# Performance work log

Measured on AMD Instinct MI355X. Metric: run time of the kernel, lower is better.

Reference implementation:

```python
import jax, jax.numpy as jnp
import numpy as np

N_NODES = 8192
N_EDGES = 524288
D_IN = 256
D_OUT = 256


def setup_inputs() -> dict:
    key = jax.random.key(0)
    ks = jax.random.split(key, 8)
    h = jax.random.normal(ks[0], (N_NODES, D_IN), dtype=jnp.float32)
    # Xavier-uniform-like scale for weights
    s = (6.0 / (D_IN + D_OUT)) ** 0.5
    W = jax.random.uniform(ks[1], (D_IN, D_OUT), jnp.float32, -s, s)
    Wq = jax.random.uniform(ks[2], (D_IN, D_OUT), jnp.float32, -s, s)
    bq = jnp.zeros((D_OUT,), jnp.float32)
    Wk = jax.random.uniform(ks[3], (D_IN, D_OUT), jnp.float32, -s, s)
    bk = jnp.zeros((D_OUT,), jnp.float32)
    senders = jax.random.randint(ks[4], (N_EDGES,), 0, N_NODES, dtype=jnp.int64 if jax.config.jax_enable_x64 else jnp.int32)
    receivers = jax.random.randint(ks[5], (N_EDGES,), 0, N_NODES, dtype=jnp.int64 if jax.config.jax_enable_x64 else jnp.int32)
    return {"h": h, "W": W, "Wq": Wq, "bq": bq, "Wk": Wk, "bk": bk,
            "senders": senders, "receivers": receivers}


def reference(h, W, Wq, bq, Wk, bk, senders, receivers):
    # Projected node features: (N, D_OUT)
    h_proj = jnp.dot(h, W)
    # Dense attention logits a = q @ k^T: (N, N), as in the original module
    q = jnp.dot(h, Wq) + bq
    k = jnp.dot(h, Wk) + bk
    a = jnp.dot(q, k.T)
    # Gather per-edge messages and attention weights, weight, scatter-add
    messages = h_proj[senders] * a[senders, receivers][:, None]  # (E, D_OUT)
    aggregated = jax.ops.segment_sum(messages, receivers, num_segments=h.shape[0])
    return jax.nn.relu(aggregated)
```

## Files before the change

kernel.cpp:

```cpp
#include <hip/hip_runtime.h>
#include <stdint.h>

typedef unsigned short u16;
typedef unsigned int u32;
typedef short v8s __attribute__((ext_vector_type(8)));
typedef float v4f __attribute__((ext_vector_type(4)));

#define N_NODES 8192
#define N_EDGES 524288
#define DFEAT 256
#define PAD 160

static __device__ __forceinline__ float bflo(u32 u) { return __uint_as_float(u << 16); }
static __device__ __forceinline__ float bfhi(u32 u) { return __uint_as_float(u & 0xffff0000u); }
static __device__ __forceinline__ u16 f2bf(float f) {
    u32 u = __float_as_uint(f);
    u32 r = (u + 0x7fffu + ((u >> 16) & 1u)) >> 16;
    return (u16)r;
}

__global__ void prep(const float* __restrict__ h,
                     const float* __restrict__ w0, const float* __restrict__ w1,
                     const float* __restrict__ w2,
                     const int* __restrict__ recv, const int* __restrict__ send,
                     u16* __restrict__ hb, u16* __restrict__ wt,
                     int* __restrict__ cnt, int* __restrict__ es_pad) {
    __shared__ u16 t[64][65];
    int b = blockIdx.x;
    if (b < 2048) {
        int i = (b * 256 + threadIdx.x) * 4;
        float4 v = *(const float4*)(h + i);
        uint2 p;
        p.x = (u32)f2bf(v.x) | ((u32)f2bf(v.y) << 16);
        p.y = (u32)f2bf(v.z) | ((u32)f2bf(v.w) << 16);
        *(uint2*)(hb + i) = p;
    } else if (b < 2096) {
        int bb = b - 2048;
        int region = bb >> 4;
        int tile = bb & 15;
        int k0 = (tile >> 2) * 64, n0 = (tile & 3) * 64;
        const float* w = (region == 0) ? w0 : ((region == 1) ? w1 : w2);
        int tx = threadIdx.x & 63, ty = threadIdx.x >> 6;
#pragma unroll
        for (int it = 0; it < 16; it++) {
            int row = it * 4 + ty;
            t[row][tx] = f2bf(w[(k0 + row) * 256 + n0 + tx]);
        }
        __syncthreads();
        u16* o = wt + region * 65536;
#pragma unroll
        for (int it = 0; it < 16; it++) {
            int row = it * 4 + ty;
            o[(n0 + row) * 256 + k0 + tx] = t[tx][row];
        }
    } else {
        int e = (b - 2096) * 256 + threadIdx.x;
        int r = recv[e];
        int pos = atomicAdd(&cnt[r], 1);
        if (pos < PAD) es_pad[r * PAD + pos] = send[e];
    }
}

__global__ __launch_bounds__(256) void gemm_proj(
    const u16* __restrict__ h, const u16* __restrict__ wt,
    const float* __restrict__ bq, const float* __restrict__ bk,
    u16* __restrict__ hproj, u16* __restrict__ qb, u16* __restrict__ kb) {
    int wave = threadIdx.x >> 6;
    int lane = threadIdx.x & 63;
    int lm = lane & 15;
    int lq = lane >> 4;
    int m0 = blockIdx.x * 64 + wave * 16;
    int region = blockIdx.y >> 2;
    int n0b = (blockIdx.y & 3) * 64;
    const u16* wtr = wt + region * 65536;

    v4f acc[4];
#pragma unroll
    for (int nt = 0; nt < 4; nt++) acc[nt] = (v4f){0.f, 0.f, 0.f, 0.f};

    const u16* arow = h + (m0 + lm) * 256 + lq * 8;
#pragma unroll
    for (int k0 = 0; k0 < 256; k0 += 32) {
        v8s a = *(const v8s*)(arow + k0);
#pragma unroll
        for (int nt = 0; nt < 4; nt++) {
            v8s b = *(const v8s*)(wtr + (n0b + nt * 16 + lm) * 256 + k0 + lq * 8);
            acc[nt] = __builtin_amdgcn_mfma_f32_16x16x32_bf16(a, b, acc[nt], 0, 0, 0);
        }
    }

    u16* outp = (region == 0) ? hproj : ((region == 1) ? qb : kb);
    const float* bias = (region == 1) ? bq : ((region == 2) ? bk : nullptr);
#pragma unroll
    for (int nt = 0; nt < 4; nt++) {
        int n = n0b + nt * 16 + lm;
        float bv = bias ? bias[n] : 0.f;
#pragma unroll
        for (int i = 0; i < 4; i++) {
            int m = m0 + lq * 4 + i;
            outp[m * 256 + n] = f2bf(acc[nt][i] + bv);
        }
    }
}

__global__ __launch_bounds__(256) void edge_fused(
    const u16* __restrict__ qb, const u16* __restrict__ kb, const u16* __restrict__ hpb,
    const int* __restrict__ cnt, const int* __restrict__ es_pad,
    float* __restrict__ out) {
    __shared__ float sc[4][16];
    __shared__ int   ss[4][16];
    int wave = threadIdx.x >> 6;
    int lane = threadIdx.x & 63;
    int r = blockIdx.x * 4 + wave;
    int lm = lane & 15, lq = lane >> 4;
    int lh = lane & 31, half = lane >> 5;
    int colbase = lh * 8;
    int n = min(cnt[r], PAD);
    int base = r * PAD;

    v8s kf[8];
    const u16* krow = kb + r * 256 + lq * 8;
#pragma unroll
    for (int t = 0; t < 8; t++) kf[t] = *(const v8s*)(krow + t * 32);

    float a[8];
#pragma unroll
    for (int i = 0; i < 8; i++) a[i] = 0.f;

    for (int c0 = 0; c0 < n; c0 += 16) {
        int j = c0 + lm;
        if (j >= n) j = n - 1;
        int s = es_pad[base + j];
        const u16* qrow = qb + s * 256 + lq * 8;
        v4f acc = (v4f){0.f, 0.f, 0.f, 0.f};
#pragma unroll
        for (int t = 0; t < 8; t++) {
            v8s av = *(const v8s*)(qrow + t * 32);
            acc = __builtin_amdgcn_mfma_f32_16x16x32_bf16(av, kf[t], acc, 0, 0, 0);
        }
        if (lm == 0) {
#pragma unroll
            for (int i = 0; i < 4; i++) sc[wave][lq * 4 + i] = acc[i];
        }
        if (lq == 0) ss[wave][lm] = s;
        __threadfence_block();

        int m = n - c0;
        if (m >= 16) {
#pragma unroll
            for (int t0 = 0; t0 < 8; t0++) {
                int t = t0 * 2 + half;
                float p = sc[wave][t];
                int s2 = ss[wave][t];
                uint4 hv = *(const uint4*)(hpb + s2 * 256 + colbase);
                a[0] += p * bflo(hv.x); a[1] += p * bfhi(hv.x);
                a[2] += p * bflo(hv.y); a[3] += p * bfhi(hv.y);
                a[4] += p * bflo(hv.z); a[5] += p * bfhi(hv.z);
                a[6] += p * bflo(hv.w); a[7] += p * bfhi(hv.w);
            }
        } else {
            for (int t = half; t < m; t += 2) {
                float p = sc[wave][t];
                int s2 = ss[wave][t];
                uint4 hv = *(const uint4*)(hpb + s2 * 256 + colbase);
                a[0] += p * bflo(hv.x); a[1] += p * bfhi(hv.x);
                a[2] += p * bflo(hv.y); a[3] += p * bfhi(hv.y);
                a[4] += p * bflo(hv.z); a[5] += p * bfhi(hv.z);
                a[6] += p * bflo(hv.w); a[7] += p * bfhi(hv.w);
            }
        }
    }

#pragma unroll
    for (int i = 0; i < 8; i++) a[i] += __shfl_xor(a[i], 32, 64);

    if (half == 0) {
        float4 o0, o1;
        o0.x = fmaxf(a[0], 0.f); o0.y = fmaxf(a[1], 0.f);
        o0.z = fmaxf(a[2], 0.f); o0.w = fmaxf(a[3], 0.f);
        o1.x = fmaxf(a[4], 0.f); o1.y = fmaxf(a[5], 0.f);
        o1.z = fmaxf(a[6], 0.f); o1.w = fmaxf(a[7], 0.f);
        float* op = out + r * 256 + colbase;
        *(float4*)op = o0;
        *(float4*)(op + 4) = o1;
    }
}

extern "C" void kernel_launch(void* const* d_in, const int* in_sizes, int n_in,
                              void* d_out, int out_size, void* d_ws, size_t ws_size,
                              hipStream_t stream) {
    const float* h  = (const float*)d_in[0];
    const float* W  = (const float*)d_in[1];
    const float* Wq = (const float*)d_in[2];
    const float* bq = (const float*)d_in[3];
    const float* Wk = (const float*)d_in[4];
    const float* bk = (const float*)d_in[5];
    const int* senders   = (const int*)d_in[6];
    const int* receivers = (const int*)d_in[7];
    float* out = (float*)d_out;

    char* ws = (char*)d_ws;
    u16* wt     = (u16*)ws;
    u16* hb     = (u16*)(ws + 393216);
    u16* hproj  = hb + N_NODES * DFEAT;
    u16* qb     = hproj + N_NODES * DFEAT;
    u16* kb     = qb + N_NODES * DFEAT;
    int* cnt    = (int*)(kb + N_NODES * DFEAT);
    int* es_pad = cnt + N_NODES;

    hipMemsetAsync(cnt, 0, N_NODES * sizeof(int), stream);
    prep<<<4144, 256, 0, stream>>>(h, W, Wq, Wk, receivers, senders, hb, wt, cnt, es_pad);
    gemm_proj<<<dim3(128, 12), 256, 0, stream>>>(hb, wt, bq, bk, hproj, qb, kb);
    edge_fused<<<N_NODES / 4, 256, 0, stream>>>(qb, kb, hproj, cnt, es_pad, out);
}
```

Measured before the change: 181.5 us.

## Restructure pipeline: fuse bucketing with GEMM, drop memset, scalar edge dot products

The memset is replaced by zeroing inside a small weight-transpose kernel. The edge bucketing is merged into the projection GEMM launch, and the GEMM now converts fp32 h to bf16 on the fly instead of using a separate hb buffer. Sender indices are stored as 16-bit values in the padded bucket array, and the edge kernel computes each q·k dot product with per-lane FMAs and shuffle reductions instead of MFMA plus shared memory. It also prefetches the next chunk of indices. Fewer launches and less memory traffic are the goal, at the cost of more ALU and shuffle work per edge. The GEMM blocks also now re-read fp32 h once per region tile.

Result: slower. 289.1 us (+59.3%).

```diff
diff --git a/kernel.cpp b/kernel.cpp
--- a/kernel.cpp
+++ b/kernel.cpp
@@ -9,35 +9,22 @@
 #define N_NODES 8192
 #define N_EDGES 524288
 #define DFEAT 256
-#define PAD 160
+#define PADC 160
 
 static __device__ __forceinline__ float bflo(u32 u) { return __uint_as_float(u << 16); }
 static __device__ __forceinline__ float bfhi(u32 u) { return __uint_as_float(u & 0xffff0000u); }
 static __device__ __forceinline__ u16 f2bf(float f) {
     u32 u = __float_as_uint(f);
-    u32 r = (u + 0x7fffu + ((u >> 16) & 1u)) >> 16;
-    return (u16)r;
-}
-
-__global__ void prep(const float* __restrict__ h,
-                     const float* __restrict__ w0, const float* __restrict__ w1,
-                     const float* __restrict__ w2,
-                     const int* __restrict__ recv, const int* __restrict__ send,
-                     u16* __restrict__ hb, u16* __restrict__ wt,
-                     int* __restrict__ cnt, int* __restrict__ es_pad) {
-    __shared__ u16 t[64][65];
+    return (u16)((u + 0x7fffu + ((u >> 16) & 1u)) >> 16);
+}
+
+__global__ void prep_small(const float* __restrict__ w0, const float* __restrict__ w1,
+                           const float* __restrict__ w2, u16* __restrict__ wt,
+                           int* __restrict__ cnt) {
     int b = blockIdx.x;
-    if (b < 2048) {
-        int i = (b * 256 + threadIdx.x) * 4;
-        float4 v = *(const float4*)(h + i);
-        uint2 p;
-        p.x = (u32)f2bf(v.x) | ((u32)f2bf(v.y) << 16);
-        p.y = (u32)f2bf(v.z) | ((u32)f2bf(v.w) << 16);
-        *(uint2*)(hb + i) = p;
-    } else if (b < 2096) {
-        int bb = b - 2048;
-        int region = bb >> 4;
-        int tile = bb & 15;
+    if (b < 48) {
+        __shared__ u16 t[64][65];
+        int region = b >> 4, tile = b & 15;
         int k0 = (tile >> 2) * 64, n0 = (tile & 3) * 64;
         const float* w = (region == 0) ? w0 : ((region == 1) ? w1 : w2);
         int tx = threadIdx.x & 63, ty = threadIdx.x >> 6;
@@ -54,133 +41,146 @@
             o[(n0 + row) * 256 + k0 + tx] = t[tx][row];
         }
     } else {
-        int e = (b - 2096) * 256 + threadIdx.x;
-        int r = recv[e];
-        int pos = atomicAdd(&cnt[r], 1);
-        if (pos < PAD) es_pad[r * PAD + pos] = send[e];
-    }
-}
-
-__global__ __launch_bounds__(256) void gemm_proj(
-    const u16* __restrict__ h, const u16* __restrict__ wt,
+        int i = ((b - 48) * 256 + threadIdx.x) * 4;
+        *(int4*)(cnt + i) = make_int4(0, 0, 0, 0);
+    }
+}
+
+__global__ __launch_bounds__(256) void main_mid(
+    const float* __restrict__ h, const u16* __restrict__ wt,
     const float* __restrict__ bq, const float* __restrict__ bk,
-    u16* __restrict__ hproj, u16* __restrict__ qb, u16* __restrict__ kb) {
-    int wave = threadIdx.x >> 6;
-    int lane = threadIdx.x & 63;
-    int lm = lane & 15;
-    int lq = lane >> 4;
-    int m0 = blockIdx.x * 64 + wave * 16;
-    int region = blockIdx.y >> 2;
-    int n0b = (blockIdx.y & 3) * 64;
-    const u16* wtr = wt + region * 65536;
-
-    v4f acc[4];
-#pragma unroll
-    for (int nt = 0; nt < 4; nt++) acc[nt] = (v4f){0.f, 0.f, 0.f, 0.f};
-
-    const u16* arow = h + (m0 + lm) * 256 + lq * 8;
-#pragma unroll
-    for (int k0 = 0; k0 < 256; k0 += 32) {
-        v8s a = *(const v8s*)(arow + k0);
+    const int* __restrict__ recv, const int* __restrict__ send,
+    u16* __restrict__ hproj, u16* __restrict__ qbuf, u16* __restrict__ kbuf,
+    int* __restrict__ cnt, u16* __restrict__ es) {
+    int b = blockIdx.x;
+    if (b < 512) {
+        int e = (b * 256 + threadIdx.x) * 4;
+        int4 rv = *(const int4*)(recv + e);
+        int4 sv = *(const int4*)(send + e);
+        int r, s, pos;
+        r = rv.x; s = sv.x; pos = atomicAdd(&cnt[r], 1); if (pos < PADC) es[r * PADC + pos] = (u16)s;
+        r = rv.y; s = sv.y; pos = atomicAdd(&cnt[r], 1); if (pos < PADC) es[r * PADC + pos] = (u16)s;
+        r = rv.z; s = sv.z; pos = atomicAdd(&cnt[r], 1); if (pos < PADC) es[r * PADC + pos] = (u16)s;
+        r = rv.w; s = sv.w; pos = atomicAdd(&cnt[r], 1); if (pos < PADC) es[r * PADC + pos] = (u16)s;
+    } else {
+        int g = b - 512;
+        int wave = threadIdx.x >> 6, lane = threadIdx.x & 63;
+        int lm = lane & 15, lq = lane >> 4;
+        int bx = g & 127, by = g >> 7;
+        int m0 = bx * 64 + wave * 16;
+        int region = by >> 2, n0b = (by & 3) * 64;
+        const u16* wtr = wt + region * 65536;
+
+        v4f acc[4];
+#pragma unroll
+        for (int nt = 0; nt < 4; nt++) acc[nt] = (v4f){0.f, 0.f, 0.f, 0.f};
+
+        const float* arow = h + (m0 + lm) * 256 + lq * 8;
+#pragma unroll
+        for (int k0 = 0; k0 < 256; k0 += 32) {
+            float4 f0 = *(const float4*)(arow + k0);
+            float4 f1 = *(const float4*)(arow + k0 + 4);
+            v8s a;
+            a[0] = (short)f2bf(f0.x); a[1] = (short)f2bf(f0.y);
+            a[2] = (short)f2bf(f0.z); a[3] = (short)f2bf(f0.w);
+            a[4] = (short)f2bf(f1.x); a[5] = (short)f2bf(f1.y);
+            a[6] = (short)f2bf(f1.z); a[7] = (short)f2bf(f1.w);
+#pragma unroll
+            for (int nt = 0; nt < 4; nt++) {
+                v8s bb = *(const v8s*)(wtr + (n0b + nt * 16 + lm) * 256 + k0 + lq * 8);
+                acc[nt] = __builtin_amdgcn_mfma_f32_16x16x32_bf16(a, bb, acc[nt], 0, 0, 0);
+            }
+        }
+        u16* outp = (region == 0) ? hproj : ((region == 1) ? qbuf : kbuf);
+        const float* bias = (region == 1) ? bq : ((region == 2) ? bk : nullptr);
 #pragma unroll
         for (int nt = 0; nt < 4; nt++) {
-            v8s b = *(const v8s*)(wtr + (n0b + nt * 16 + lm) * 256 + k0 + lq * 8);
-            acc[nt] = __builtin_amdgcn_mfma_f32_16x16x32_bf16(a, b, acc[nt], 0, 0, 0);
-        }
-    }
-
-    u16* outp = (region == 0) ? hproj : ((region == 1) ? qb : kb);
-    const float* bias = (region == 1) ? bq : ((region == 2) ? bk : nullptr);
-#pragma unroll
-    for (int nt = 0; nt < 4; nt++) {
-        int n = n0b + nt * 16 + lm;
-        float bv = bias ? bias[n] : 0.f;
-#pragma unroll
-        for (int i = 0; i < 4; i++) {
-            int m = m0 + lq * 4 + i;
-            outp[m * 256 + n] = f2bf(acc[nt][i] + bv);
-        }
-    }
-}
-
-__global__ __launch_bounds__(256) void edge_fused(
-    const u16* __restrict__ qb, const u16* __restrict__ kb, const u16* __restrict__ hpb,
-    const int* __restrict__ cnt, const int* __restrict__ es_pad,
-    float* __restrict__ out) {
-    __shared__ float sc[4][16];
-    __shared__ int   ss[4][16];
-    int wave = threadIdx.x >> 6;
-    int lane = threadIdx.x & 63;
+            int nn = n0b + nt * 16 + lm;
+            float bv = bias ? bias[nn] : 0.f;
+#pragma unroll
+            for (int i = 0; i < 4; i++) {
+                int m = m0 + lq * 4 + i;
+                outp[m * 256 + nn] = f2bf(acc[nt][i] + bv);
+            }
+        }
+    }
+}
+
+#define DOT_AGG(SW, T) do {                                                   \
+    int s_ = (int)(((SW) >> (((T) & 1) * 16)) & 0xffffu);                     \
+    int off_ = s_ * 256 + cb;                                                 \
+    uint4 qv_ = *(const uint4*)(qbuf + off_);                                 \
+    uint4 hv_ = *(const uint4*)(hpb + off_);                                  \
+    float p_ = kr0 * bflo(qv_.x) + kr1 * bfhi(qv_.x)                          \
+             + kr2 * bflo(qv_.y) + kr3 * bfhi(qv_.y)                          \
+             + kr4 * bflo(qv_.z) + kr5 * bfhi(qv_.z)                          \
+             + kr6 * bflo(qv_.w) + kr7 * bfhi(qv_.w);                         \
+    p_ += __shfl_xor(p_, 1, 32);                                              \
+    p_ += __shfl_xor(p_, 2, 32);                                              \
+    p_ += __shfl_xor(p_, 4, 32);                                              \
+    p_ += __shfl_xor(p_, 8, 32);                                              \
+    p_ += __shfl_xor(p_, 16, 32);                                             \
+    a0 += p_ * bflo(hv_.x); a1 += p_ * bfhi(hv_.x);                           \
+    a2 += p_ * bflo(hv_.y); a3 += p_ * bfhi(hv_.y);                           \
+    a4 += p_ * bflo(hv_.z); a5 += p_ * bfhi(hv_.z);                           \
+    a6 += p_ * bflo(hv_.w); a7 += p_ * bfhi(hv_.w);                           \
+} while (0)
+
+__global__ __launch_bounds__(256, 8) void edge_fused(
+    const u16* __restrict__ qbuf, const u16* __restrict__ kbuf,
+    const u16* __restrict__ hpb, const int* __restrict__ cnt,
+    const u16* __restrict__ es, float* __restrict__ out) {
+    int wave = threadIdx.x >> 6, lane = threadIdx.x & 63;
     int r = blockIdx.x * 4 + wave;
-    int lm = lane & 15, lq = lane >> 4;
     int lh = lane & 31, half = lane >> 5;
-    int colbase = lh * 8;
-    int n = min(cnt[r], PAD);
-    int base = r * PAD;
-
-    v8s kf[8];
-    const u16* krow = kb + r * 256 + lq * 8;
-#pragma unroll
-    for (int t = 0; t < 8; t++) kf[t] = *(const v8s*)(krow + t * 32);
-
-    float a[8];
-#pragma unroll
-    for (int i = 0; i < 8; i++) a[i] = 0.f;
-
+    int cb = lh * 8;
+    int n = min(cnt[r], PADC);
+    int base = r * PADC;
+
+    uint4 kv = *(const uint4*)(kbuf + r * 256 + cb);
+    float kr0 = bflo(kv.x), kr1 = bfhi(kv.x), kr2 = bflo(kv.y), kr3 = bfhi(kv.y),
+          kr4 = bflo(kv.z), kr5 = bfhi(kv.z), kr6 = bflo(kv.w), kr7 = bfhi(kv.w);
+
+    float a0 = 0.f, a1 = 0.f, a2 = 0.f, a3 = 0.f,
+          a4 = 0.f, a5 = 0.f, a6 = 0.f, a7 = 0.f;
+
+    uint4 sp = *(const uint4*)(es + base + half * 8);
     for (int c0 = 0; c0 < n; c0 += 16) {
-        int j = c0 + lm;
-        if (j >= n) j = n - 1;
-        int s = es_pad[base + j];
-        const u16* qrow = qb + s * 256 + lq * 8;
-        v4f acc = (v4f){0.f, 0.f, 0.f, 0.f};
-#pragma unroll
-        for (int t = 0; t < 8; t++) {
-            v8s av = *(const v8s*)(qrow + t * 32);
-            acc = __builtin_amdgcn_mfma_f32_16x16x32_bf16(av, kf[t], acc, 0, 0, 0);
-        }
-        if (lm == 0) {
-#pragma unroll
-            for (int i = 0; i < 4; i++) sc[wave][lq * 4 + i] = acc[i];
-        }
-        if (lq == 0) ss[wave][lm] = s;
-        __threadfence_block();
-
-        int m = n - c0;
-        if (m >= 16) {
-#pragma unroll
-            for (int t0 = 0; t0 < 8; t0++) {
-                int t = t0 * 2 + half;
-                float p = sc[wave][t];
-                int s2 = ss[wave][t];
-                uint4 hv = *(const uint4*)(hpb + s2 * 256 + colbase);
-                a[0] += p * bflo(hv.x); a[1] += p * bfhi(hv.x);
-                a[2] += p * bflo(hv.y); a[3] += p * bfhi(hv.y);
-                a[4] += p * bflo(hv.z); a[5] += p * bfhi(hv.z);
-                a[6] += p * bflo(hv.w); a[7] += p * bfhi(hv.w);
-            }
+        int nx = c0 + 16;
+        uint4 spn = sp;
+        if (nx < n) spn = *(const uint4*)(es + base + nx + half * 8);
+
+        if (nx <= n) {
+            DOT_AGG(sp.x, 0); DOT_AGG(sp.x, 1);
+            DOT_AGG(sp.y, 2); DOT_AGG(sp.y, 3);
+            DOT_AGG(sp.z, 4); DOT_AGG(sp.z, 5);
+            DOT_AGG(sp.w, 6); DOT_AGG(sp.w, 7);
         } else {
-            for (int t = half; t < m; t += 2) {
-                float p = sc[wave][t];
-                int s2 = ss[wave][t];
-                uint4 hv = *(const uint4*)(hpb + s2 * 256 + colbase);
-                a[0] += p * bflo(hv.x); a[1] += p * bfhi(hv.x);
-                a[2] += p * bflo(hv.y); a[3] += p * bfhi(hv.y);
-                a[4] += p * bflo(hv.z); a[5] += p * bfhi(hv.z);
-                a[6] += p * bflo(hv.w); a[7] += p * bfhi(hv.w);
-            }
-        }
-    }
-
-#pragma unroll
-    for (int i = 0; i < 8; i++) a[i] += __shfl_xor(a[i], 32, 64);
+            int mrem = n - (c0 + half * 8);
+            if (0 < mrem) DOT_AGG(sp.x, 0);
+            if (1 < mrem) DOT_AGG(sp.x, 1);
+            if (2 < mrem) DOT_AGG(sp.y, 2);
+            if (3 < mrem) DOT_AGG(sp.y, 3);
+            if (4 < mrem) DOT_AGG(sp.z, 4);
+            if (5 < mrem) DOT_AGG(sp.z, 5);
+            if (6 < mrem) DOT_AGG(sp.w, 6);
+            if (7 < mrem) DOT_AGG(sp.w, 7);
+        }
+        sp = spn;
+    }
+
+    a0 += __shfl_xor(a0, 32, 64); a1 += __shfl_xor(a1, 32, 64);
+    a2 += __shfl_xor(a2, 32, 64); a3 += __shfl_xor(a3, 32, 64);
+    a4 += __shfl_xor(a4, 32, 64); a5 += __shfl_xor(a5, 32, 64);
+    a6 += __shfl_xor(a6, 32, 64); a7 += __shfl_xor(a7, 32, 64);
 
     if (half == 0) {
         float4 o0, o1;
-        o0.x = fmaxf(a[0], 0.f); o0.y = fmaxf(a[1], 0.f);
-        o0.z = fmaxf(a[2], 0.f); o0.w = fmaxf(a[3], 0.f);
-        o1.x = fmaxf(a[4], 0.f); o1.y = fmaxf(a[5], 0.f);
-        o1.z = fmaxf(a[6], 0.f); o1.w = fmaxf(a[7], 0.f);
-        float* op = out + r * 256 + colbase;
+        o0.x = fmaxf(a0, 0.f); o0.y = fmaxf(a1, 0.f);
+        o0.z = fmaxf(a2, 0.f); o0.w = fmaxf(a3, 0.f);
+        o1.x = fmaxf(a4, 0.f); o1.y = fmaxf(a5, 0.f);
+        o1.z = fmaxf(a6, 0.f); o1.w = fmaxf(a7, 0.f);
+        float* op = out + r * 256 + cb;
         *(float4*)op = o0;
         *(float4*)(op + 4) = o1;
     }
@@ -200,16 +200,15 @@
     float* out = (float*)d_out;
 
     char* ws = (char*)d_ws;
-    u16* wt     = (u16*)ws;
-    u16* hb     = (u16*)(ws + 393216);
-    u16* hproj  = hb + N_NODES * DFEAT;
-    u16* qb     = hproj + N_NODES * DFEAT;
-    u16* kb     = qb + N_NODES * DFEAT;
-    int* cnt    = (int*)(kb + N_NODES * DFEAT);
-    int* es_pad = cnt + N_NODES;
-
-    hipMemsetAsync(cnt, 0, N_NODES * sizeof(int), stream);
-    prep<<<4144, 256, 0, stream>>>(h, W, Wq, Wk, receivers, senders, hb, wt, cnt, es_pad);
-    gemm_proj<<<dim3(128, 12), 256, 0, stream>>>(hb, wt, bq, bk, hproj, qb, kb);
-    edge_fused<<<N_NODES / 4, 256, 0, stream>>>(qb, kb, hproj, cnt, es_pad, out);
-}
+    u16* wt    = (u16*)ws;
+    u16* hproj = (u16*)(ws + 393216);
+    u16* qbuf  = hproj + N_NODES * DFEAT;
+    u16* kbuf  = qbuf + N_NODES * DFEAT;
+    int* cnt   = (int*)(kbuf + N_NODES * DFEAT);
+    u16* es    = (u16*)(cnt + N_NODES);
+
+    prep_small<<<56, 256, 0, stream>>>(W, Wq, Wk, wt, cnt);
+    main_mid<<<2048, 256, 0, stream>>>(h, wt, bq, bk, receivers, senders,
+                                       hproj, qbuf, kbuf, cnt, es);
+    edge_fused<<<N_NODES / 4, 256, 0, stream>>>(qbuf, kbuf, hproj, cnt, es, out);
+}
```
